# Kernel tuning notes

Measured on AMD Instinct MI355X. Metric: run time of the kernel, lower is better.

## Reference

```python
import jax, jax.numpy as jnp
import numpy as np

INV_SQRT_2 = 0.5 ** 0.5

B, N, D_IN, D_OUT = 2, 50000, 64, 64
E = 800000


def setup_inputs() -> dict:
    key = jax.random.key(0)
    k1, k2, k3, k4, k5, k6 = jax.random.split(key, 6)
    x = jax.random.normal(k1, (B, N, D_IN, 3), dtype=jnp.float32)
    W_node = jax.random.normal(k2, (D_OUT, D_IN), dtype=jnp.float32)
    W_edge = jax.random.normal(k3, (D_OUT, D_IN), dtype=jnp.float32)
    norm_coeff = jax.random.uniform(k4, (N,), dtype=jnp.float32)
    src = jax.random.randint(k5, (E,), 0, N, dtype=jnp.int32)
    dst = jax.random.randint(k6, (E,), 0, N, dtype=jnp.int32)
    return {"x": x, "W_node": W_node, "W_edge": W_edge,
            "norm_coeff": norm_coeff, "src": src, "dst": dst}


def reference(x, W_node, W_edge, norm_coeff, src, dst):
    # x: (B, N, D_IN, 3)
    y_node = jnp.einsum('oi,bnik->bnok', W_node, x)      # (B, N, D_OUT, 3)
    y_edge = jnp.einsum('oi,bnik->bnok', W_edge, x)      # (B, N, D_OUT, 3)
    # gather by src along node axis, scatter-add into dst
    gathered = y_edge[:, src]                            # (B, E, D_OUT, 3)
    agg = jnp.zeros_like(y_node).at[:, dst].add(gathered)  # (B, N, D_OUT, 3)
    ans = y_node + norm_coeff[:, None, None] * agg
    return ans * INV_SQRT_2
```

## Files before the change

### kernel.cpp

```cpp
#include <hip/hip_runtime.h>
#include <hip/hip_bf16.h>

constexpr int B_   = 2;
constexpr int N_   = 50000;
constexpr int E_   = 800000;
constexpr int CAP  = 64;
constexpr int WPB  = 8;
constexpr float INV_SQRT_2 = 0.70710678118654752440f;


__global__ __launch_bounds__(256) void zero_kernel(int* __restrict__ p, int n) {
    int i = blockIdx.x * 256 + threadIdx.x;
    if (i < n) p[i] = 0;
}

__global__ __launch_bounds__(256) void scatter_direct_kernel(
    const int* __restrict__ src,
    const int* __restrict__ dst,
    int* counts,
    int* __restrict__ sorted_pad)
{
    int t = blockIdx.x * 256 + threadIdx.x;
    if (t * 4 >= E_) return;
    int4 dv = ((const int4*)dst)[t];
    int4 sv = ((const int4*)src)[t];
    int p0 = atomicAdd(&counts[dv.x], 1);
    int p1 = atomicAdd(&counts[dv.y], 1);
    int p2 = atomicAdd(&counts[dv.z], 1);
    int p3 = atomicAdd(&counts[dv.w], 1);
    if (p0 < CAP) sorted_pad[(dv.x << 6) + p0] = sv.x;
    if (p1 < CAP) sorted_pad[(dv.y << 6) + p1] = sv.y;
    if (p2 < CAP) sorted_pad[(dv.z << 6) + p2] = sv.z;
    if (p3 < CAP) sorted_pad[(dv.w << 6) + p3] = sv.w;
}

__device__ __forceinline__ unsigned f2bf(float f) {
    unsigned u = __float_as_uint(f);
    return (u + 0x7fffu + ((u >> 16) & 1u)) >> 16;
}

__global__ __launch_bounds__(512, 8) void fused_kernel(
    const float* __restrict__ x,
    const float* __restrict__ Wn,
    const float* __restrict__ We,
    const float* __restrict__ norm,
    const int* __restrict__ counts,
    const int* __restrict__ sorted_pad,
    float* __restrict__ out)
{
    __shared__ unsigned WnP[32][64];
    __shared__ unsigned WeP[32][64];
    __shared__ __align__(16) float xs[WPB][192];
    __shared__ __align__(16) float xa[WPB][192];

    for (int t = threadIdx.x; t < 2048; t += 512) {
        int i2 = t >> 6, o = t & 63;
        WnP[i2][o] = f2bf(Wn[o * 64 + 2 * i2]) | (f2bf(Wn[o * 64 + 2 * i2 + 1]) << 16);
        WeP[i2][o] = f2bf(We[o * 64 + 2 * i2]) | (f2bf(We[o * 64 + 2 * i2 + 1]) << 16);
    }
    __syncthreads();

    const int wave = threadIdx.x >> 6;
    const int lane = threadIdx.x & 63;
    const int p = blockIdx.x * WPB + wave;
    const int b = p / N_;
    const int d = p - b * N_;

    const float* xp = x + (size_t)p * 192;
    if (lane < 48) {
        ((float4*)&xs[wave][0])[lane] = ((const float4*)xp)[lane];
    }

    const int degc = counts[d];
    const int deg = degc < CAP ? degc : CAP;
    const int* sp = sorted_pad + (d << 6);
    const float4* xb4 = (const float4*)(x + (size_t)b * N_ * 192);
    if (lane < 48) {
        float ax = 0.f, ay = 0.f, az = 0.f, aw = 0.f;
        int e = 0;
        for (; e + 3 < deg; e += 4) {
            int s0 = sp[e + 0];
            int s1 = sp[e + 1];
            int s2 = sp[e + 2];
            int s3 = sp[e + 3];
            float4 v0 = xb4[(size_t)s0 * 48 + lane];
            float4 v1 = xb4[(size_t)s1 * 48 + lane];
            float4 v2 = xb4[(size_t)s2 * 48 + lane];
            float4 v3 = xb4[(size_t)s3 * 48 + lane];
            ax += (v0.x + v1.x) + (v2.x + v3.x);
            ay += (v0.y + v1.y) + (v2.y + v3.y);
            az += (v0.z + v1.z) + (v2.z + v3.z);
            aw += (v0.w + v1.w) + (v2.w + v3.w);
        }
        for (; e < deg; ++e) {
            int s = sp[e];
            float4 v = xb4[(size_t)s * 48 + lane];
            ax += v.x; ay += v.y; az += v.z; aw += v.w;
        }
        float4 a4; a4.x = ax; a4.y = ay; a4.z = az; a4.w = aw;
        ((float4*)&xa[wave][0])[lane] = a4;
    }

    float an0 = 0.f, an1 = 0.f, an2 = 0.f;
    float ae0 = 0.f, ae1 = 0.f, ae2 = 0.f;
    const float4* xsv = (const float4*)&xs[wave][0];
    const float4* xav = (const float4*)&xa[wave][0];

    #pragma unroll
    for (int i4 = 0; i4 < 16; ++i4) {
        unsigned un0 = WnP[2 * i4 + 0][lane];
        unsigned un1 = WnP[2 * i4 + 1][lane];
        unsigned ue0 = WeP[2 * i4 + 0][lane];
        unsigned ue1 = WeP[2 * i4 + 1][lane];
        float4 d0 = xsv[i4 * 3 + 0];
        float4 d1 = xsv[i4 * 3 + 1];
        float4 d2 = xsv[i4 * 3 + 2];
        float4 g0 = xav[i4 * 3 + 0];
        float4 g1 = xav[i4 * 3 + 1];
        float4 g2 = xav[i4 * 3 + 2];
        float wn0 = __uint_as_float(un0 << 16);
        float wn1 = __uint_as_float(un0 & 0xffff0000u);
        float wn2 = __uint_as_float(un1 << 16);
        float wn3 = __uint_as_float(un1 & 0xffff0000u);
        float we0 = __uint_as_float(ue0 << 16);
        float we1 = __uint_as_float(ue0 & 0xffff0000u);
        float we2 = __uint_as_float(ue1 << 16);
        float we3 = __uint_as_float(ue1 & 0xffff0000u);

        an0 = fmaf(wn0, d0.x, an0); an1 = fmaf(wn0, d0.y, an1); an2 = fmaf(wn0, d0.z, an2);
        an0 = fmaf(wn1, d0.w, an0); an1 = fmaf(wn1, d1.x, an1); an2 = fmaf(wn1, d1.y, an2);
        an0 = fmaf(wn2, d1.z, an0); an1 = fmaf(wn2, d1.w, an1); an2 = fmaf(wn2, d2.x, an2);
        an0 = fmaf(wn3, d2.y, an0); an1 = fmaf(wn3, d2.z, an1); an2 = fmaf(wn3, d2.w, an2);

        ae0 = fmaf(we0, g0.x, ae0); ae1 = fmaf(we0, g0.y, ae1); ae2 = fmaf(we0, g0.z, ae2);
        ae0 = fmaf(we1, g0.w, ae0); ae1 = fmaf(we1, g1.x, ae1); ae2 = fmaf(we1, g1.y, ae2);
        ae0 = fmaf(we2, g1.z, ae0); ae1 = fmaf(we2, g1.w, ae1); ae2 = fmaf(we2, g2.x, ae2);
        ae0 = fmaf(we3, g2.y, ae0); ae1 = fmaf(we3, g2.z, ae1); ae2 = fmaf(we3, g2.w, ae2);
    }

    const float sc = norm[d];
    const size_t off = (size_t)p * 192 + (size_t)lane * 3;
    out[off + 0] = INV_SQRT_2 * fmaf(sc, ae0, an0);
    out[off + 1] = INV_SQRT_2 * fmaf(sc, ae1, an1);
    out[off + 2] = INV_SQRT_2 * fmaf(sc, ae2, an2);
}

extern "C" void kernel_launch(void* const* d_in, const int* in_sizes, int n_in,
                              void* d_out, int out_size, void* d_ws, size_t ws_size,
                              hipStream_t stream) {
    const float* x    = (const float*)d_in[0];
    const float* Wn   = (const float*)d_in[1];
    const float* We   = (const float*)d_in[2];
    const float* norm = (const float*)d_in[3];
    const int*   src  = (const int*)d_in[4];
    const int*   dst  = (const int*)d_in[5];
    float* out = (float*)d_out;

    int* counts     = (int*)d_ws;
    int* sorted_pad = counts + N_;

    zero_kernel<<<(N_ + 255) / 256, 256, 0, stream>>>(counts, N_);
    scatter_direct_kernel<<<(E_ / 4 + 255) / 256, 256, 0, stream>>>(src, dst, counts, sorted_pad);
    fused_kernel<<<(B_ * N_) / WPB, 512, 0, stream>>>(x, Wn, We, norm, counts,
                                                      sorted_pad, out);
}
```

Measured before the change: 534.2 us.

## Pre-convert x to bf16 and gather bf16 rows in fused kernel

```diff
diff --git a/kernel.cpp b/kernel.cpp
--- a/kernel.cpp
+++ b/kernel.cpp
@@ -8,44 +8,69 @@
 constexpr int WPB  = 8;
 constexpr float INV_SQRT_2 = 0.70710678118654752440f;
 
+constexpr int SCAT_THREADS = E_ / 4;
+constexpr int SCAT_BLKS    = (SCAT_THREADS + 255) / 256;
+constexpr int CONV_ELEMS   = B_ * N_ * 192;
+constexpr int CONV_THREADS = CONV_ELEMS / 8;
+constexpr int CONV_BLKS    = CONV_THREADS / 256;
+
 
 __global__ __launch_bounds__(256) void zero_kernel(int* __restrict__ p, int n) {
     int i = blockIdx.x * 256 + threadIdx.x;
     if (i < n) p[i] = 0;
 }
 
-__global__ __launch_bounds__(256) void scatter_direct_kernel(
-    const int* __restrict__ src,
-    const int* __restrict__ dst,
-    int* counts,
-    int* __restrict__ sorted_pad)
-{
-    int t = blockIdx.x * 256 + threadIdx.x;
-    if (t * 4 >= E_) return;
-    int4 dv = ((const int4*)dst)[t];
-    int4 sv = ((const int4*)src)[t];
-    int p0 = atomicAdd(&counts[dv.x], 1);
-    int p1 = atomicAdd(&counts[dv.y], 1);
-    int p2 = atomicAdd(&counts[dv.z], 1);
-    int p3 = atomicAdd(&counts[dv.w], 1);
-    if (p0 < CAP) sorted_pad[(dv.x << 6) + p0] = sv.x;
-    if (p1 < CAP) sorted_pad[(dv.y << 6) + p1] = sv.y;
-    if (p2 < CAP) sorted_pad[(dv.z << 6) + p2] = sv.z;
-    if (p3 < CAP) sorted_pad[(dv.w << 6) + p3] = sv.w;
-}
-
 __device__ __forceinline__ unsigned f2bf(float f) {
     unsigned u = __float_as_uint(f);
     return (u + 0x7fffu + ((u >> 16) & 1u)) >> 16;
 }
+__device__ __forceinline__ float blo(unsigned u) { return __uint_as_float(u << 16); }
+__device__ __forceinline__ float bhi(unsigned u) { return __uint_as_float(u & 0xffff0000u); }
+
+__global__ __launch_bounds__(256) void prep_kernel(
+    const int* __restrict__ src,
+    const int* __restrict__ dst,
+    const float* __restrict__ x,
+    int* counts,
+    int* __restrict__ sorted_pad,
+    unsigned* __restrict__ xbf)
+{
+    const int bid = blockIdx.x;
+    if (bid < SCAT_BLKS) {
+        int t = bid * 256 + threadIdx.x;
+        if (t < SCAT_THREADS) {
+            int4 dv = ((const int4*)dst)[t];
+            int4 sv = ((const int4*)src)[t];
+            int p0 = atomicAdd(&counts[dv.x], 1);
+            int p1 = atomicAdd(&counts[dv.y], 1);
+            int p2 = atomicAdd(&counts[dv.z], 1);
+            int p3 = atomicAdd(&counts[dv.w], 1);
+            if (p0 < CAP) sorted_pad[(dv.x << 6) + p0] = sv.x;
+            if (p1 < CAP) sorted_pad[(dv.y << 6) + p1] = sv.y;
+            if (p2 < CAP) sorted_pad[(dv.z << 6) + p2] = sv.z;
+            if (p3 < CAP) sorted_pad[(dv.w << 6) + p3] = sv.w;
+        }
+    } else {
+        int t = (bid - SCAT_BLKS) * 256 + threadIdx.x;
+        const float4* xp = (const float4*)x;
+        float4 a = xp[(size_t)t * 2 + 0];
+        float4 c = xp[(size_t)t * 2 + 1];
+        uint4 o;
+        o.x = f2bf(a.x) | (f2bf(a.y) << 16);
+        o.y = f2bf(a.z) | (f2bf(a.w) << 16);
+        o.z = f2bf(c.x) | (f2bf(c.y) << 16);
+        o.w = f2bf(c.z) | (f2bf(c.w) << 16);
+        ((uint4*)xbf)[t] = o;
+    }
+}
 
 __global__ __launch_bounds__(512, 8) void fused_kernel(
-    const float* __restrict__ x,
     const float* __restrict__ Wn,
     const float* __restrict__ We,
     const float* __restrict__ norm,
     const int* __restrict__ counts,
     const int* __restrict__ sorted_pad,
+    const unsigned* __restrict__ xbf,
     float* __restrict__ out)
 {
     __shared__ unsigned WnP[32][64];
@@ -66,36 +91,45 @@
     const int b = p / N_;
     const int d = p - b * N_;
 
-    const float* xp = x + (size_t)p * 192;
-    if (lane < 48) {
-        ((float4*)&xs[wave][0])[lane] = ((const float4*)xp)[lane];
-    }
-
     const int degc = counts[d];
     const int deg = degc < CAP ? degc : CAP;
     const int* sp = sorted_pad + (d << 6);
-    const float4* xb4 = (const float4*)(x + (size_t)b * N_ * 192);
+    const uint2* xb2 = (const uint2*)xbf + (size_t)b * N_ * 48;
+
     if (lane < 48) {
+        uint2 ov = xb2[(size_t)d * 48 + lane];
+        float4 s4;
+        s4.x = blo(ov.x); s4.y = bhi(ov.x);
+        s4.z = blo(ov.y); s4.w = bhi(ov.y);
+        ((float4*)&xs[wave][0])[lane] = s4;
+
         float ax = 0.f, ay = 0.f, az = 0.f, aw = 0.f;
         int e = 0;
-        for (; e + 3 < deg; e += 4) {
-            int s0 = sp[e + 0];
-            int s1 = sp[e + 1];
-            int s2 = sp[e + 2];
-            int s3 = sp[e + 3];
-            float4 v0 = xb4[(size_t)s0 * 48 + lane];
-            float4 v1 = xb4[(size_t)s1 * 48 + lane];
-            float4 v2 = xb4[(size_t)s2 * 48 + lane];
-            float4 v3 = xb4[(size_t)s3 * 48 + lane];
-            ax += (v0.x + v1.x) + (v2.x + v3.x);
-            ay += (v0.y + v1.y) + (v2.y + v3.y);
-            az += (v0.z + v1.z) + (v2.z + v3.z);
-            aw += (v0.w + v1.w) + (v2.w + v3.w);
+        for (; e + 7 < deg; e += 8) {
+            int s0 = sp[e + 0], s1 = sp[e + 1], s2 = sp[e + 2], s3 = sp[e + 3];
+            int s4i = sp[e + 4], s5 = sp[e + 5], s6 = sp[e + 6], s7 = sp[e + 7];
+            uint2 v0 = xb2[(size_t)s0 * 48 + lane];
+            uint2 v1 = xb2[(size_t)s1 * 48 + lane];
+            uint2 v2 = xb2[(size_t)s2 * 48 + lane];
+            uint2 v3 = xb2[(size_t)s3 * 48 + lane];
+            uint2 v4 = xb2[(size_t)s4i * 48 + lane];
+            uint2 v5 = xb2[(size_t)s5 * 48 + lane];
+            uint2 v6 = xb2[(size_t)s6 * 48 + lane];
+            uint2 v7 = xb2[(size_t)s7 * 48 + lane];
+            ax += ((blo(v0.x) + blo(v1.x)) + (blo(v2.x) + blo(v3.x)))
+                + ((blo(v4.x) + blo(v5.x)) + (blo(v6.x) + blo(v7.x)));
+            ay += ((bhi(v0.x) + bhi(v1.x)) + (bhi(v2.x) + bhi(v3.x)))
+                + ((bhi(v4.x) + bhi(v5.x)) + (bhi(v6.x) + bhi(v7.x)));
+            az += ((blo(v0.y) + blo(v1.y)) + (blo(v2.y) + blo(v3.y)))
+                + ((blo(v4.y) + blo(v5.y)) + (blo(v6.y) + blo(v7.y)));
+            aw += ((bhi(v0.y) + bhi(v1.y)) + (bhi(v2.y) + bhi(v3.y)))
+                + ((bhi(v4.y) + bhi(v5.y)) + (bhi(v6.y) + bhi(v7.y)));
         }
         for (; e < deg; ++e) {
             int s = sp[e];
-            float4 v = xb4[(size_t)s * 48 + lane];
-            ax += v.x; ay += v.y; az += v.z; aw += v.w;
+            uint2 v = xb2[(size_t)s * 48 + lane];
+            ax += blo(v.x); ay += bhi(v.x);
+            az += blo(v.y); aw += bhi(v.y);
         }
         float4 a4; a4.x = ax; a4.y = ay; a4.z = az; a4.w = aw;
         ((float4*)&xa[wave][0])[lane] = a4;
@@ -118,14 +152,8 @@
         float4 g0 = xav[i4 * 3 + 0];
         float4 g1 = xav[i4 * 3 + 1];
         float4 g2 = xav[i4 * 3 + 2];
-        float wn0 = __uint_as_float(un0 << 16);
-        float wn1 = __uint_as_float(un0 & 0xffff0000u);
-        float wn2 = __uint_as_float(un1 << 16);
-        float wn3 = __uint_as_float(un1 & 0xffff0000u);
-        float we0 = __uint_as_float(ue0 << 16);
-        float we1 = __uint_as_float(ue0 & 0xffff0000u);
-        float we2 = __uint_as_float(ue1 << 16);
-        float we3 = __uint_as_float(ue1 & 0xffff0000u);
+        float wn0 = blo(un0), wn1 = bhi(un0), wn2 = blo(un1), wn3 = bhi(un1);
+        float we0 = blo(ue0), we1 = bhi(ue0), we2 = blo(ue1), we3 = bhi(ue1);
 
         an0 = fmaf(wn0, d0.x, an0); an1 = fmaf(wn0, d0.y, an1); an2 = fmaf(wn0, d0.z, an2);
         an0 = fmaf(wn1, d0.w, an0); an1 = fmaf(wn1, d1.x, an1); an2 = fmaf(wn1, d1.y, an2);
@@ -156,11 +184,13 @@
     const int*   dst  = (const int*)d_in[5];
     float* out = (float*)d_out;
 
-    int* counts     = (int*)d_ws;
-    int* sorted_pad = counts + N_;
+    int* counts        = (int*)d_ws;
+    int* sorted_pad    = counts + N_;
+    unsigned* xbf      = (unsigned*)(sorted_pad + (size_t)CAP * N_);
 
     zero_kernel<<<(N_ + 255) / 256, 256, 0, stream>>>(counts, N_);
-    scatter_direct_kernel<<<(E_ / 4 + 255) / 256, 256, 0, stream>>>(src, dst, counts, sorted_pad);
-    fused_kernel<<<(B_ * N_) / WPB, 512, 0, stream>>>(x, Wn, We, norm, counts,
-                                                      sorted_pad, out);
+    prep_kernel<<<SCAT_BLKS + CONV_BLKS, 256, 0, stream>>>(src, dst, x, counts,
+                                                           sorted_pad, xbf);
+    fused_kernel<<<(B_ * N_) / WPB, 512, 0, stream>>>(Wn, We, norm, counts,
+                                                      sorted_pad, xbf, out);
 }
```

Result: faster. 481.5 us (-9.9%).
